# Optimization experiments

Measured on AMD Instinct MI355X. Metric: run time of the kernel, lower is better.

The kernel has to match this reference:

```python
import jax, jax.numpy as jnp
import numpy as np

N_NODES = 50000
N_EDGES = 1600000
IN_CH = 512
OUT_CH = 64
ITERATIONS = 3


def _spmm(adj_index, adj_values, x):
    # sparse @ dense: out[r] = sum_{e: row[e]==r} vals[e] * x[col[e]]
    row, col = adj_index[0], adj_index[1]
    gathered = adj_values[:, None] * x[col]  # [E, F]
    return jax.ops.segment_sum(gathered, row, num_segments=x.shape[0])


def setup_inputs() -> dict:
    key = jax.random.key(0)
    k1, k2, k3, k4, k5 = jax.random.split(key, 5)
    adj_index = jax.random.randint(k1, (2, N_EDGES), 0, N_NODES, dtype=jnp.int64)
    # positive normalized-like edge weights ~ 1/avg_degree
    adj_values = jax.random.uniform(k2, (N_EDGES,), dtype=jnp.float32) / 32.0
    features = jax.random.normal(k3, (N_NODES, IN_CH), dtype=jnp.float32)
    xavier_w = float(np.sqrt(6.0 / (IN_CH + OUT_CH)))
    weight_matrix = jax.random.uniform(k4, (IN_CH, OUT_CH), dtype=jnp.float32, minval=-xavier_w, maxval=xavier_w)
    xavier_b = float(np.sqrt(6.0 / (1 + OUT_CH)))
    bias = jax.random.uniform(k5, (1, OUT_CH), dtype=jnp.float32, minval=-xavier_b, maxval=xavier_b)
    return {"adj_index": adj_index, "adj_values": adj_values, "features": features,
            "weight_matrix": weight_matrix, "bias": bias}


def reference(adj_index, adj_values, features, weight_matrix, bias):
    # dense projection (dropout_rate=0.0 / eval mode -> identity dropout)
    base = features @ weight_matrix  # [N, OUT_CH]
    # repeated sparse-dense propagation: A^(iterations-1) @ (X W)
    for _ in range(ITERATIONS - 1):
        base = _spmm(adj_index, adj_values, base)
    return base + bias
```

## Files before the change

### kernel.cpp

```cpp
#include <hip/hip_runtime.h>
#include <hip/hip_bf16.h>

typedef __attribute__((ext_vector_type(8))) __bf16 bf16x8;
typedef __attribute__((ext_vector_type(4))) float f32x4;

#define IN_CH 512
#define OUT_CH 64
#define BS 98
#define NB 512
#define CHUNK 8192
#define CAP 4096

__device__ inline unsigned short f2bf(float f) {
    __hip_bfloat16 h = __float2bfloat16(f);
    return __builtin_bit_cast(unsigned short, h);
}
__device__ inline float bf2f(unsigned short u) {
    return __uint_as_float(((unsigned)u) << 16);
}

__global__ __launch_bounds__(512) void prep_kernel(
    const float* __restrict__ W, __hip_bfloat16* __restrict__ Wf,
    int* __restrict__ bcur)
{
    const int t = blockIdx.x * 512 + threadIdx.x;
    if (t < NB) bcur[t] = t * CAP;
    const int ct = t >> 10;
    const int rem = t & 1023;
    const int ks = rem >> 6;
    const int l = rem & 63;
    const int col = ct * 16 + (l & 15);
    const int kb = ks * 32 + (l >> 4) * 8;
    __hip_bfloat16* dst = Wf + (size_t)t * 8;
    #pragma unroll
    for (int j = 0; j < 8; ++j)
        dst[j] = (__hip_bfloat16)W[(size_t)(kb + j) * OUT_CH + col];
}

__global__ __launch_bounds__(128) void gemm_kernel(
    const float* __restrict__ A, const bf16x8* __restrict__ wf,
    __hip_bfloat16* __restrict__ outb, int N)
{
    __shared__ __align__(16) char Abf[32 * 1024];

    const int tid = threadIdx.x;
    const int row0 = blockIdx.x * 32;

    #pragma unroll 1
    for (int ob = 0; ob < 4; ++ob) {
        float4 v[8];
        #pragma unroll
        for (int j = 0; j < 8; ++j) {
            int f = (ob * 8 + j) * 128 + tid;
            int row = f >> 7, c4 = f & 127;
            int rg = row0 + row; rg = rg < N ? rg : N - 1;
            v[j] = *(const float4*)(A + (size_t)rg * IN_CH + c4 * 4);
        }
        #pragma unroll
        for (int j = 0; j < 8; ++j) {
            int f = (ob * 8 + j) * 128 + tid;
            int row = f >> 7, c4 = f & 127;
            int blk = c4 >> 1, half = c4 & 1;
            ushort4 h;
            h.x = f2bf(v[j].x); h.y = f2bf(v[j].y);
            h.z = f2bf(v[j].z); h.w = f2bf(v[j].w);
            *(ushort4*)(Abf + row * 1024 + ((blk ^ (row & 7)) << 4) + (half << 3)) = h;
        }
    }
    __syncthreads();

    const int lane = tid & 63;
    const int wave = tid >> 6;
    const int arow = wave * 16 + (lane & 15);
    const int kgb = lane >> 4;

    bf16x8 a[16];
    #pragma unroll
    for (int ks = 0; ks < 16; ++ks)
        a[ks] = *(const bf16x8*)(Abf + arow * 1024 +
                                 (((ks * 4 + kgb) ^ (arow & 7)) << 4));

    const int colb = lane & 15;
    const int rr = row0 + wave * 16 + (lane >> 4) * 4;
    #pragma unroll 1
    for (int ct = 0; ct < 4; ++ct) {
        bf16x8 w[16];
        #pragma unroll
        for (int ks = 0; ks < 16; ++ks) w[ks] = wf[(ct * 16 + ks) * 64 + lane];
        f32x4 acc = {0.f, 0.f, 0.f, 0.f};
        #pragma unroll
        for (int ks = 0; ks < 16; ++ks)
            acc = __builtin_amdgcn_mfma_f32_16x16x32_bf16(a[ks], w[ks], acc, 0, 0, 0);
        int col = ct * 16 + colb;
        #pragma unroll
        for (int i = 0; i < 4; ++i) {
            int r = rr + i;
            if (r < N)
                outb[(size_t)r * OUT_CH + col] = __float2bfloat16(acc[i]);
        }
    }
}

__global__ __launch_bounds__(512) void bucket_scatter_kernel(
    const int* __restrict__ rows, const int* __restrict__ cols,
    const float* __restrict__ vals, int* __restrict__ bcur,
    int2* __restrict__ seg, int E)
{
    __shared__ int hist[NB];
    __shared__ int posBase[NB];
    const int tid = threadIdx.x;
    const int base = blockIdx.x * CHUNK + tid * 16;

    hist[tid] = 0;
    __syncthreads();

    int myb[16], mypack[16]; float myval[16];
    if (base + 16 <= E) {
        int4 r4[4], c4[4]; float4 v4[4];
        #pragma unroll
        for (int q = 0; q < 4; ++q) {
            r4[q] = *(const int4*)(rows + base + q * 4);
            c4[q] = *(const int4*)(cols + base + q * 4);
            v4[q] = *(const float4*)(vals + base + q * 4);
        }
        #pragma unroll
        for (int q = 0; q < 4; ++q) {
            int rr[4] = {r4[q].x, r4[q].y, r4[q].z, r4[q].w};
            int cc[4] = {c4[q].x, c4[q].y, c4[q].z, c4[q].w};
            float vv[4] = {v4[q].x, v4[q].y, v4[q].z, v4[q].w};
            #pragma unroll
            for (int u = 0; u < 4; ++u) {
                int j = q * 4 + u;
                int r = rr[u];
                int b = r / BS;
                myb[j] = b;
                mypack[j] = (cc[u] << 8) | (r - b * BS);
                myval[j] = vv[u];
                atomicAdd(&hist[b], 1);
            }
        }
    } else {
        #pragma unroll
        for (int j = 0; j < 16; ++j) {
            int e = base + j;
            myb[j] = -1;
            if (e < E) {
                int r = rows[e];
                int b = r / BS;
                myb[j] = b;
                mypack[j] = (cols[e] << 8) | (r - b * BS);
                myval[j] = vals[e];
                atomicAdd(&hist[b], 1);
            }
        }
    }
    __syncthreads();

    int h = hist[tid];
    if (h) posBase[tid] = atomicAdd(&bcur[tid], h);
    hist[tid] = 0;
    __syncthreads();

    #pragma unroll
    for (int j = 0; j < 16; ++j) {
        if (myb[j] >= 0) {
            int p = posBase[myb[j]] + atomicAdd(&hist[myb[j]], 1);
            int2 cv; cv.x = mypack[j]; cv.y = __float_as_int(myval[j]);
            seg[p] = cv;
        }
    }
}

__global__ __launch_bounds__(512) void sort_kernel(
    const int* __restrict__ bcur, const int2* __restrict__ seg,
    unsigned* __restrict__ segc,
    int* __restrict__ offs, int* __restrict__ rend)
{
    __shared__ unsigned sorted4[CAP];
    __shared__ int hist[BS + 1];
    __shared__ int cursor[BS];

    const int b = blockIdx.x;
    const int t = threadIdx.x;
    const int s = b * CAP;
    const int cnt = bcur[b] - s;

    if (t < BS + 1) hist[t] = 0;
    __syncthreads();

    int2 ed[8];
    #pragma unroll
    for (int j = 0; j < 8; ++j) {
        int idx = t + j * 512;
        if (idx < cnt) {
            ed[j] = seg[s + idx];
            atomicAdd(&hist[ed[j].x & 255], 1);
        }
    }
    __syncthreads();

    if (t == 0) {
        int run = 0;
        for (int i = 0; i < BS; ++i) { int c = hist[i]; hist[i] = run; run += c; }
        hist[BS] = run;
    }
    __syncthreads();

    if (t < BS) {
        cursor[t] = hist[t];
        offs[b * BS + t] = s + hist[t];
        rend[b * BS + t] = s + hist[t + 1];
    }
    __syncthreads();

    #pragma unroll
    for (int j = 0; j < 8; ++j) {
        int idx = t + j * 512;
        if (idx < cnt) {
            int pos = atomicAdd(&cursor[ed[j].x & 255], 1);
            unsigned col = ((unsigned)ed[j].x) >> 8;
            sorted4[pos] = (col << 16) | f2bf(__int_as_float(ed[j].y));
        }
    }
    __syncthreads();

    #pragma unroll
    for (int j = 0; j < 8; ++j) {
        int idx = t + j * 512;
        if (idx < cnt) segc[s + idx] = sorted4[idx];
    }
}

__global__ __launch_bounds__(256) void spmm_row_kernel(
    const int* __restrict__ offs, const int* __restrict__ rend,
    const unsigned* __restrict__ segc,
    const __hip_bfloat16* __restrict__ x,
    __hip_bfloat16* __restrict__ yb,
    float* __restrict__ yf,
    const float* __restrict__ bias, int N)
{
    const int tid = threadIdx.x;
    const int lane = tid & 63;
    const int wave = tid >> 6;
    const int grp = lane >> 4;
    const int l16 = lane & 15;

    int r = (blockIdx.x * 4 + wave) * 4 + grp;
    const bool rv = r < N;
    const int rc = rv ? r : N - 1;
    const int s = offs[rc];
    const int e = rv ? rend[rc] : s;

    int m = e - s;
    m = max(m, __shfl_xor(m, 16));
    m = max(m, __shfl_xor(m, 32));
    const int iters = (m + 15) >> 4;

    const ushort* xp = (const ushort*)x + l16 * 4;

    float4 acc = {0.f, 0.f, 0.f, 0.f};
    for (int it = 0; it < iters; ++it) {
        const int base = s + it * 16;
        unsigned p[16];
        #pragma unroll
        for (int j = 0; j < 16; ++j) {
            int idx = base + j;
            p[j] = segc[idx < e ? idx : s];
        }
        ushort4 xv[16];
        #pragma unroll
        for (int j = 0; j < 16; ++j)
            xv[j] = *(const ushort4*)(xp + (size_t)(p[j] >> 16) * OUT_CH);
        #pragma unroll
        for (int j = 0; j < 16; ++j) {
            int idx = base + j;
            float wv = (idx < e) ? __uint_as_float(p[j] << 16) : 0.f;
            acc.x = fmaf(wv, bf2f(xv[j].x), acc.x);
            acc.y = fmaf(wv, bf2f(xv[j].y), acc.y);
            acc.z = fmaf(wv, bf2f(xv[j].z), acc.z);
            acc.w = fmaf(wv, bf2f(xv[j].w), acc.w);
        }
    }

    if (rv) {
        if (yf) {
            float4 bv = *(const float4*)(bias + l16 * 4);
            float4 o;
            o.x = acc.x + bv.x; o.y = acc.y + bv.y;
            o.z = acc.z + bv.z; o.w = acc.w + bv.w;
            *(float4*)(yf + (size_t)r * OUT_CH + l16 * 4) = o;
        } else {
            ushort4 h;
            h.x = f2bf(acc.x); h.y = f2bf(acc.y);
            h.z = f2bf(acc.z); h.w = f2bf(acc.w);
            *(ushort4*)((ushort*)yb + (size_t)r * OUT_CH + l16 * 4) = h;
        }
    }
}

static inline size_t align_up(size_t v) { return (v + 255) & ~(size_t)255; }

extern "C" void kernel_launch(void* const* d_in, const int* in_sizes, int n_in,
                              void* d_out, int out_size, void* d_ws, size_t ws_size,
                              hipStream_t stream)
{
    const int*   adj  = (const int*)d_in[0];
    const float* vals = (const float*)d_in[1];
    const float* feat = (const float*)d_in[2];
    const float* Wm   = (const float*)d_in[3];
    const float* bias = (const float*)d_in[4];

    const int E = in_sizes[1];
    const int N = in_sizes[2] / IN_CH;
    const int* rows  = adj;
    const int* colsI = adj + E;

    char* w = (char*)d_ws;
    size_t o = 0;
    __hip_bfloat16* B0b = (__hip_bfloat16*)(w + o); o += align_up((size_t)N * OUT_CH * 2);
    __hip_bfloat16* Y1b = (__hip_bfloat16*)(w + o); o += align_up((size_t)N * OUT_CH * 2);
    __hip_bfloat16* Wf  = (__hip_bfloat16*)(w + o); o += align_up((size_t)IN_CH * OUT_CH * 2);
    int*      bcur = (int*)     (w + o); o += align_up(NB * sizeof(int));
    int*      offs = (int*)     (w + o); o += align_up((size_t)NB * BS * sizeof(int));
    int*      rend = (int*)     (w + o); o += align_up((size_t)NB * BS * sizeof(int));
    int2*     seg  = (int2*)    (w + o); o += align_up((size_t)NB * CAP * sizeof(int2));
    unsigned* segc = (unsigned*)(w + o); o += align_up((size_t)NB * CAP * sizeof(unsigned));
    (void)ws_size; (void)n_in; (void)out_size;

    prep_kernel<<<8, 512, 0, stream>>>(Wm, Wf, bcur);

    gemm_kernel<<<(N + 31) / 32, 128, 0, stream>>>(
        feat, (const bf16x8*)Wf, B0b, N);

    bucket_scatter_kernel<<<(E + CHUNK - 1) / CHUNK, 512, 0, stream>>>(
        rows, colsI, vals, bcur, seg, E);
    sort_kernel<<<NB, 512, 0, stream>>>(bcur, seg, segc, offs, rend);

    const int rows_per_block = 16;
    spmm_row_kernel<<<(N + rows_per_block - 1) / rows_per_block, 256, 0, stream>>>(
        offs, rend, segc, B0b, Y1b, nullptr, nullptr, N);
    spmm_row_kernel<<<(N + rows_per_block - 1) / rows_per_block, 256, 0, stream>>>(
        offs, rend, segc, Y1b, nullptr, (float*)d_out, bias, N);
}
```

Measured before the change: 117.8 us.

## Fuse first SpMM into bucket sort kernel and prefetch GEMM input loads

The first sparse propagation now runs inside the sort kernel, reading the sorted edges straight from shared memory. This removes one kernel launch and a global re-read of the compacted edge list and row offsets. The GEMM staging loop also double-buffers its global loads, fetching the next chunk before converting the current one. The fused kernel relies on hist holding row prefix offsets after the sort, and it adds register pressure and longer-running sort blocks.

```diff
diff --git a/kernel.cpp b/kernel.cpp
--- a/kernel.cpp
+++ b/kernel.cpp
@@ -46,15 +46,24 @@
     const int tid = threadIdx.x;
     const int row0 = blockIdx.x * 32;
 
+    float4 v[8], vn[8];
+    #pragma unroll
+    for (int j = 0; j < 8; ++j) {
+        int f = j * 128 + tid;
+        int row = f >> 7, c4 = f & 127;
+        int rg = row0 + row; rg = rg < N ? rg : N - 1;
+        v[j] = *(const float4*)(A + (size_t)rg * IN_CH + c4 * 4);
+    }
     #pragma unroll 1
     for (int ob = 0; ob < 4; ++ob) {
-        float4 v[8];
-        #pragma unroll
-        for (int j = 0; j < 8; ++j) {
-            int f = (ob * 8 + j) * 128 + tid;
-            int row = f >> 7, c4 = f & 127;
-            int rg = row0 + row; rg = rg < N ? rg : N - 1;
-            v[j] = *(const float4*)(A + (size_t)rg * IN_CH + c4 * 4);
+        if (ob < 3) {
+            #pragma unroll
+            for (int j = 0; j < 8; ++j) {
+                int f = ((ob + 1) * 8 + j) * 128 + tid;
+                int row = f >> 7, c4 = f & 127;
+                int rg = row0 + row; rg = rg < N ? rg : N - 1;
+                vn[j] = *(const float4*)(A + (size_t)rg * IN_CH + c4 * 4);
+            }
         }
         #pragma unroll
         for (int j = 0; j < 8; ++j) {
@@ -66,6 +75,8 @@
             h.z = f2bf(v[j].z); h.w = f2bf(v[j].w);
             *(ushort4*)(Abf + row * 1024 + ((blk ^ (row & 7)) << 4) + (half << 3)) = h;
         }
+        #pragma unroll
+        for (int j = 0; j < 8; ++j) v[j] = vn[j];
     }
     __syncthreads();
 
@@ -171,10 +182,12 @@
     }
 }
 
-__global__ __launch_bounds__(512) void sort_kernel(
+__global__ __launch_bounds__(512) void sortspmm_kernel(
     const int* __restrict__ bcur, const int2* __restrict__ seg,
     unsigned* __restrict__ segc,
-    int* __restrict__ offs, int* __restrict__ rend)
+    int* __restrict__ offs, int* __restrict__ rend,
+    const __hip_bfloat16* __restrict__ x,
+    __hip_bfloat16* __restrict__ y1, int N)
 {
     __shared__ unsigned sorted4[CAP];
     __shared__ int hist[BS + 1];
@@ -229,15 +242,57 @@
         int idx = t + j * 512;
         if (idx < cnt) segc[s + idx] = sorted4[idx];
     }
+
+    const int lane = t & 63;
+    const int wave = t >> 6;
+    const int grp = lane >> 4;
+    const int l16 = lane & 15;
+    const ushort* xp = (const ushort*)x + l16 * 4;
+
+    #pragma unroll 1
+    for (int sweep = 0; sweep < 4; ++sweep) {
+        int rr = sweep * 32 + wave * 4 + grp;
+        int rrc = rr < BS ? rr : BS - 1;
+        int rs = hist[rrc];
+        int re = hist[rrc + 1];
+        int gr = b * BS + rr;
+        if (rr >= BS || gr >= N) re = rs;
+
+        float4 acc = {0.f, 0.f, 0.f, 0.f};
+        for (int i0 = rs; i0 < re; i0 += 16) {
+            unsigned p[16];
+            #pragma unroll
+            for (int j = 0; j < 16; ++j) {
+                int idx = i0 + j;
+                p[j] = sorted4[idx < re ? idx : rs];
+            }
+            ushort4 xv[16];
+            #pragma unroll
+            for (int j = 0; j < 16; ++j)
+                xv[j] = *(const ushort4*)(xp + (size_t)(p[j] >> 16) * OUT_CH);
+            #pragma unroll
+            for (int j = 0; j < 16; ++j) {
+                float wv = (i0 + j < re) ? __uint_as_float(p[j] << 16) : 0.f;
+                acc.x = fmaf(wv, bf2f(xv[j].x), acc.x);
+                acc.y = fmaf(wv, bf2f(xv[j].y), acc.y);
+                acc.z = fmaf(wv, bf2f(xv[j].z), acc.z);
+                acc.w = fmaf(wv, bf2f(xv[j].w), acc.w);
+            }
+        }
+        if (rr < BS && gr < N) {
+            ushort4 h;
+            h.x = f2bf(acc.x); h.y = f2bf(acc.y);
+            h.z = f2bf(acc.z); h.w = f2bf(acc.w);
+            *(ushort4*)((ushort*)y1 + (size_t)gr * OUT_CH + l16 * 4) = h;
+        }
+    }
 }
 
 __global__ __launch_bounds__(256) void spmm_row_kernel(
     const int* __restrict__ offs, const int* __restrict__ rend,
     const unsigned* __restrict__ segc,
     const __hip_bfloat16* __restrict__ x,
-    __hip_bfloat16* __restrict__ yb,
-    float* __restrict__ yf,
-    const float* __restrict__ bias, int N)
+    float* __restrict__ yf, const float* __restrict__ bias, int N)
 {
     const int tid = threadIdx.x;
     const int lane = tid & 63;
@@ -283,18 +338,11 @@
     }
 
     if (rv) {
-        if (yf) {
-            float4 bv = *(const float4*)(bias + l16 * 4);
-            float4 o;
-            o.x = acc.x + bv.x; o.y = acc.y + bv.y;
-            o.z = acc.z + bv.z; o.w = acc.w + bv.w;
-            *(float4*)(yf + (size_t)r * OUT_CH + l16 * 4) = o;
-        } else {
-            ushort4 h;
-            h.x = f2bf(acc.x); h.y = f2bf(acc.y);
-            h.z = f2bf(acc.z); h.w = f2bf(acc.w);
-            *(ushort4*)((ushort*)yb + (size_t)r * OUT_CH + l16 * 4) = h;
-        }
+        float4 bv = *(const float4*)(bias + l16 * 4);
+        float4 o;
+        o.x = acc.x + bv.x; o.y = acc.y + bv.y;
+        o.z = acc.z + bv.z; o.w = acc.w + bv.w;
+        *(float4*)(yf + (size_t)r * OUT_CH + l16 * 4) = o;
     }
 }
 
@@ -334,11 +382,10 @@
 
     bucket_scatter_kernel<<<(E + CHUNK - 1) / CHUNK, 512, 0, stream>>>(
         rows, colsI, vals, bcur, seg, E);
-    sort_kernel<<<NB, 512, 0, stream>>>(bcur, seg, segc, offs, rend);
-
-    const int rows_per_block = 16;
-    spmm_row_kernel<<<(N + rows_per_block - 1) / rows_per_block, 256, 0, stream>>>(
-        offs, rend, segc, B0b, Y1b, nullptr, nullptr, N);
-    spmm_row_kernel<<<(N + rows_per_block - 1) / rows_per_block, 256, 0, stream>>>(
-        offs, rend, segc, Y1b, nullptr, (float*)d_out, bias, N);
-}
+
+    sortspmm_kernel<<<NB, 512, 0, stream>>>(
+        bcur, seg, segc, offs, rend, B0b, Y1b, N);
+
+    spmm_row_kernel<<<(N + 15) / 16, 256, 0, stream>>>(
+        offs, rend, segc, Y1b, (float*)d_out, bias, N);
+}
```

After: 113.4 us. -3.7%, faster.
